# Performance work log

Hardware: AMD Instinct MI355X
Metric: run time of the kernel (lower is better)

Reference implementation:

```python
import jax, jax.numpy as jnp
import numpy as np

NUM_GRAPHS = 64
LEAKY_SLOPE = 0.2
LN_EPS = 1e-5


def setup_inputs() -> dict:
    key = jax.random.key(0)
    ks = jax.random.split(key, 32)
    N, E = 100000, 1600000
    H, C, D = 4, 32, 128
    L = 4
    inp = {}
    inp['x'] = jax.random.normal(ks[0], (N, 8), dtype=jnp.float32)
    inp['edge_index'] = jax.random.randint(ks[1], (2, E), 0, N, dtype=jnp.int64)
    inp['edge_attr'] = jax.random.normal(ks[2], (E, 3), dtype=jnp.float32)
    inp['batch'] = jnp.sort(jax.random.randint(ks[3], (N,), 0, NUM_GRAPHS, dtype=jnp.int64))
    s = 0.05
    inp['node_w'] = jax.random.normal(ks[4], (8, D), dtype=jnp.float32) * s
    inp['node_b'] = jax.random.normal(ks[5], (D,), dtype=jnp.float32) * s
    inp['edge_w'] = jax.random.normal(ks[6], (3, D), dtype=jnp.float32) * s
    inp['edge_b'] = jax.random.normal(ks[7], (D,), dtype=jnp.float32) * s
    inp['gat_lin'] = jax.random.normal(ks[8], (L, D, D), dtype=jnp.float32) * s
    inp['gat_att_src'] = jax.random.normal(ks[9], (L, H, C), dtype=jnp.float32) * s
    inp['gat_att_dst'] = jax.random.normal(ks[10], (L, H, C), dtype=jnp.float32) * s
    inp['gat_lin_edge'] = jax.random.normal(ks[11], (L, D, D), dtype=jnp.float32) * s
    inp['gat_att_edge'] = jax.random.normal(ks[12], (L, H, C), dtype=jnp.float32) * s
    inp['gat_bias'] = jax.random.normal(ks[13], (L, D), dtype=jnp.float32) * s
    inp['ln_g'] = jnp.ones((L, D), dtype=jnp.float32)
    inp['ln_b'] = jnp.zeros((L, D), dtype=jnp.float32)
    inp['dos_w1'] = jax.random.normal(ks[14], (D, D // 2), dtype=jnp.float32) * s
    inp['dos_b1'] = jax.random.normal(ks[15], (D // 2,), dtype=jnp.float32) * s
    inp['dos_w2'] = jax.random.normal(ks[16], (D // 2, 100), dtype=jnp.float32) * s
    inp['dos_b2'] = jax.random.normal(ks[17], (100,), dtype=jnp.float32) * s
    inp['trans_w1'] = jax.random.normal(ks[18], (D, D // 2), dtype=jnp.float32) * s
    inp['trans_b1'] = jax.random.normal(ks[19], (D // 2,), dtype=jnp.float32) * s
    inp['trans_w2'] = jax.random.normal(ks[20], (D // 2, 100), dtype=jnp.float32) * s
    inp['trans_b2'] = jax.random.normal(ks[21], (100,), dtype=jnp.float32) * s
    return inp


def _gat_layer(x, ea, src, dst, lin, a_s, a_d, lin_e, a_e, bias):
    # PyG GATConv (concat=True, add_self_loops=True, fill_value='mean'), eval mode.
    N = x.shape[0]
    H, C = a_s.shape
    h = (x @ lin).reshape(N, H, C)            # [N,H,C]
    # add self loops; self-loop edge_attr = mean of edge_attr over edges
    loop = jnp.arange(N, dtype=src.dtype)
    src_f = jnp.concatenate([src, loop])
    dst_f = jnp.concatenate([dst, loop])
    ea_mean = jnp.broadcast_to(ea.mean(axis=0), (N, ea.shape[1]))
    ea_f = jnp.concatenate([ea, ea_mean], axis=0)
    e = (ea_f @ lin_e).reshape(-1, H, C)      # [E+N,H,C]
    a_src = (h * a_s).sum(-1)                 # [N,H]
    a_dst = (h * a_d).sum(-1)                 # [N,H]
    alpha = a_src[src_f] + a_dst[dst_f] + (e * a_e).sum(-1)  # [E+N,H]
    alpha = jnp.where(alpha >= 0, alpha, LEAKY_SLOPE * alpha)
    # segment softmax over destination nodes
    m = jax.ops.segment_max(alpha, dst_f, num_segments=N)
    ex = jnp.exp(alpha - m[dst_f])
    denom = jax.ops.segment_sum(ex, dst_f, num_segments=N)
    w = ex / (denom[dst_f] + 1e-16)           # [E+N,H]
    msg = h[src_f] * w[:, :, None]            # [E+N,H,C]
    out = jax.ops.segment_sum(msg, dst_f, num_segments=N)
    return out.reshape(N, H * C) + bias


def _layer_norm(x, g, b):
    mu = x.mean(-1, keepdims=True)
    var = ((x - mu) ** 2).mean(-1, keepdims=True)
    return (x - mu) * jax.lax.rsqrt(var + LN_EPS) * g + b


def reference(x, edge_index, edge_attr, batch, node_w, node_b, edge_w, edge_b,
              gat_lin, gat_att_src, gat_att_dst, gat_lin_edge, gat_att_edge,
              gat_bias, ln_g, ln_b, dos_w1, dos_b1, dos_w2, dos_b2,
              trans_w1, trans_b1, trans_w2, trans_b2):
    src, dst = edge_index[0], edge_index[1]
    h = x @ node_w + node_b                   # [N,128]
    ea = edge_attr @ edge_w + edge_b          # [E,128]
    L = gat_lin.shape[0]
    for i in range(L):
        h = _gat_layer(h, ea, src, dst, gat_lin[i], gat_att_src[i],
                       gat_att_dst[i], gat_lin_edge[i], gat_att_edge[i], gat_bias[i])
        h = _layer_norm(h, ln_g[i], ln_b[i])
        h = jax.nn.relu(h)
        # dropout is identity in eval mode
    # global mean pool over graphs
    sums = jax.ops.segment_sum(h, batch, num_segments=NUM_GRAPHS)
    cnts = jax.ops.segment_sum(jnp.ones((h.shape[0], 1), h.dtype), batch, num_segments=NUM_GRAPHS)
    g = sums / jnp.maximum(cnts, 1.0)         # [G,128]
    dos = jax.nn.relu(g @ dos_w1 + dos_b1) @ dos_w2 + dos_b2
    trans = jax.nn.relu(g @ trans_w1 + trans_b1) @ trans_w2 + trans_b2
    return (dos, trans)
```

## Files before the change

kernel.cpp:

```cpp
#include <hip/hip_runtime.h>

#define LEAKY 0.2f
#define LN_EPSV 1e-5f
#define NGRAPH 64

typedef __attribute__((ext_vector_type(8))) short short8v;
typedef __attribute__((ext_vector_type(4))) float f32x4;

static __device__ __forceinline__ float leakyf(float x){ return x >= 0.f ? x : LEAKY*x; }

static __device__ __forceinline__ unsigned short f2bf(float f){
  unsigned int u = __float_as_uint(f);
  u = (u + 0x7fffu + ((u >> 16) & 1u)) >> 16;
  return (unsigned short)u;
}
static __device__ __forceinline__ float bf2f(unsigned short v){
  return __uint_as_float(((unsigned int)v) << 16);
}

__global__ void node_encode_k(const float* __restrict__ x, const float* __restrict__ w,
                              const float* __restrict__ b, unsigned short* __restrict__ hb, int N){
  int tid = blockIdx.x*blockDim.x + threadIdx.x;
  int n = tid >> 5; int c4 = (tid & 31) * 4;
  if (n >= N) return;
  float xr[8];
  #pragma unroll
  for (int k=0;k<8;k++) xr[k] = x[(size_t)n*8+k];
  float4 acc = *(const float4*)&b[c4];
  #pragma unroll
  for (int k=0;k<8;k++){
    float4 wv = *(const float4*)&w[k*128 + c4];
    acc.x += xr[k]*wv.x; acc.y += xr[k]*wv.y; acc.z += xr[k]*wv.z; acc.w += xr[k]*wv.w;
  }
  ushort4 o; o.x=f2bf(acc.x); o.y=f2bf(acc.y); o.z=f2bf(acc.z); o.w=f2bf(acc.w);
  *(ushort4*)&hb[(size_t)n*128 + c4] = o;
}

__global__ void ea_mean_k(const float* __restrict__ ea, float* __restrict__ out, int E){
  float s0=0.f,s1=0.f,s2=0.f;
  for (int e = blockIdx.x*blockDim.x + threadIdx.x; e < E; e += gridDim.x*blockDim.x){
    s0 += ea[(size_t)e*3]; s1 += ea[(size_t)e*3+1]; s2 += ea[(size_t)e*3+2];
  }
  #pragma unroll
  for (int m=32;m;m>>=1){ s0 += __shfl_xor(s0,m); s1 += __shfl_xor(s1,m); s2 += __shfl_xor(s2,m); }
  __shared__ float ls[3][8];
  int wv = threadIdx.x>>6;
  if ((threadIdx.x&63)==0){ ls[0][wv]=s0; ls[1][wv]=s1; ls[2][wv]=s2; }
  __syncthreads();
  if (threadIdx.x==0){
    float a=0.f,b=0.f,c=0.f;
    int nw = blockDim.x>>6;
    for(int i=0;i<nw;i++){ a+=ls[0][i]; b+=ls[1][i]; c+=ls[2][i]; }
    atomicAdd(&out[0],a); atomicAdd(&out[1],b); atomicAdd(&out[2],c);
  }
}

__global__ void csr_count_k(const int* __restrict__ dst, int* __restrict__ cnt, int E){
  int e = blockIdx.x*blockDim.x + threadIdx.x;
  if (e<E) atomicAdd(&cnt[dst[e]], 1);
}

__global__ void scan1_k(const int* __restrict__ in, int* __restrict__ incl, int* __restrict__ bsum, int n){
  __shared__ int s[1024];
  int i = blockIdx.x*1024 + threadIdx.x;
  int v = (i<n)? in[i]:0;
  s[threadIdx.x]=v; __syncthreads();
  for(int off=1;off<1024;off<<=1){
    int t = (threadIdx.x>=off)? s[threadIdx.x-off] : 0;
    __syncthreads();
    s[threadIdx.x]+=t; __syncthreads();
  }
  if(i<n) incl[i]=s[threadIdx.x];
  if(threadIdx.x==1023) bsum[blockIdx.x]=s[1023];
}
__global__ void scan2_k(const int* __restrict__ bsum, int* __restrict__ boff, int nb){
  if(threadIdx.x==0 && blockIdx.x==0){
    int run=0;
    for(int i=0;i<nb;i++){ boff[i]=run; run+=bsum[i]; }
  }
}
__global__ void scan3_k(const int* __restrict__ incl, const int* __restrict__ boff, int* __restrict__ row_ptr, int n){
  int i = blockIdx.x*blockDim.x + threadIdx.x;
  if(i<n) row_ptr[i+1] = incl[i] + boff[i>>10];
  if(i==0) row_ptr[0]=0;
}

__global__ void csr_fill_k(const int* __restrict__ src, const int* __restrict__ dst,
                           const float* __restrict__ eattr,
                           const int* __restrict__ row_ptr, int* __restrict__ cnt,
                           float4* __restrict__ csr_rec, int E){
  int e = blockIdx.x*blockDim.x + threadIdx.x;
  if (e>=E) return;
  int d = dst[e];
  int pos = row_ptr[d] + atomicAdd(&cnt[d],1);
  csr_rec[pos] = make_float4(eattr[(size_t)e*3], eattr[(size_t)e*3+1], eattr[(size_t)e*3+2],
                             __int_as_float(src[e]));
}

__global__ void precompute_k(const float* __restrict__ lin_e, const float* __restrict__ a_e,
                             const float* __restrict__ edge_w, const float* __restrict__ edge_b,
                             const float* __restrict__ emean_sum, float invE,
                             float* __restrict__ params){
  int l = blockIdx.x; int t = threadIdx.x;
  __shared__ float Ve[128][4];
  __shared__ float sW3[12]; __shared__ float sce[4];
  const float* Le = lin_e + (size_t)l*16384; const float* Ae = a_e + l*128;
  #pragma unroll
  for(int h=0; h<4; h++){
    float v=0.f;
    for(int c=0;c<32;c++) v += Le[t*128 + h*32 + c]*Ae[h*32+c];
    Ve[t][h]=v;
  }
  __syncthreads();
  float* P = params + l*32;
  if(t<12){ int k=t>>2, h=t&3; float v=0.f; for(int d=0;d<128;d++) v += edge_w[k*128+d]*Ve[d][h]; P[t]=v; sW3[t]=v; }
  if(t>=16 && t<20){ int h=t-16; float v=0.f; for(int d=0;d<128;d++) v += edge_b[d]*Ve[d][h]; P[12+h]=v; sce[h]=v; }
  __syncthreads();
  if(t<4){
    float v = sce[t];
    for(int k=0;k<3;k++) v += emean_sum[k]*invE * sW3[k*4+t];
    P[16+t]=v;
  }
}

__global__ void prepack_w_k(const float* __restrict__ gat_lin, short8v* __restrict__ wpack){
  int l = blockIdx.x; int t = threadIdx.x;
  const float* W = gat_lin + (size_t)l*16384;
  for(int f = t; f < 2048; f += 256){
    int j = f >> 8, ks = (f >> 6) & 3, lane = f & 63;
    int lo = lane & 15, hi = (lane >> 4) & 3;
    short8v b;
    #pragma unroll
    for(int e=0;e<8;e++) b[e] = (short)f2bf(W[(size_t)(ks*32 + hi*8 + e)*128 + j*16 + lo]);
    wpack[(size_t)l*2048 + f] = b;
  }
}

__global__ __launch_bounds__(256) void mfma_dense_k(const unsigned short* __restrict__ hin,
    const short8v* __restrict__ wpack, const float* __restrict__ att_s, const float* __restrict__ att_d,
    unsigned short* __restrict__ hbf, float* __restrict__ a_src, float* __restrict__ a_dst,
    int N, int ntiles){
  int lane = threadIdx.x & 63;
  int wid  = threadIdx.x >> 6;
  int lo = lane & 15, hi = lane >> 4;
  short8v Bf[8][4];
  #pragma unroll
  for(int j=0;j<8;j++){
    #pragma unroll
    for(int ks=0;ks<4;ks++)
      Bf[j][ks] = wpack[(j<<8) + (ks<<6) + lane];
  }
  float as[8], ad[8];
  #pragma unroll
  for(int j=0;j<8;j++){ as[j]=att_s[j*16+lo]; ad[j]=att_d[j*16+lo]; }

  for(int t = blockIdx.x*4 + wid; t < ntiles; t += gridDim.x*4){
    int n0 = t*16;
    int arow = n0 + lo; if(arow >= N) arow = N-1;
    short8v A[4];
    #pragma unroll
    for(int ks=0;ks<4;ks++)
      A[ks] = *(const short8v*)&hin[(size_t)arow*128 + ks*32 + hi*8];
    float ps[4][4], pd[4][4];
    #pragma unroll
    for(int r=0;r<4;r++){
      #pragma unroll
      for(int h=0;h<4;h++){ ps[r][h]=0.f; pd[r][h]=0.f; }
    }
    #pragma unroll
    for(int j=0;j<8;j++){
      f32x4 acc = {0.f,0.f,0.f,0.f};
      #pragma unroll
      for(int ks=0;ks<4;ks++)
        acc = __builtin_amdgcn_mfma_f32_16x16x32_bf16(A[ks], Bf[j][ks], acc, 0, 0, 0);
      int h = j>>1;
      #pragma unroll
      for(int r=0;r<4;r++){
        int row = n0 + hi*4 + r;
        if(row < N) hbf[(size_t)row*128 + j*16 + lo] = f2bf(acc[r]);
        ps[r][h] += acc[r]*as[j];
        pd[r][h] += acc[r]*ad[j];
      }
    }
    #pragma unroll
    for(int r=0;r<4;r++){
      #pragma unroll
      for(int h=0;h<4;h++){
        #pragma unroll
        for(int msk=1; msk<16; msk<<=1){
          ps[r][h] += __shfl_xor(ps[r][h], msk);
          pd[r][h] += __shfl_xor(pd[r][h], msk);
        }
      }
    }
    if(lo==0){
      #pragma unroll
      for(int r=0;r<4;r++){
        int row = n0 + hi*4 + r;
        if(row<N){
          *(float4*)&a_src[(size_t)row*4] = make_float4(ps[r][0],ps[r][1],ps[r][2],ps[r][3]);
          *(float4*)&a_dst[(size_t)row*4] = make_float4(pd[r][0],pd[r][1],pd[r][2],pd[r][3]);
        }
      }
    }
  }
}

__global__ void aggregate_k(const unsigned int* __restrict__ hbf, const float* __restrict__ a_src,
    const float* __restrict__ a_dst, const int* __restrict__ row_ptr,
    const float4* __restrict__ csr_rec, const float* __restrict__ params,
    const float* __restrict__ bias, const float* __restrict__ lng, const float* __restrict__ lnb,
    unsigned int* __restrict__ h_out, int N){
  int lane = threadIdx.x & 63;
  int n = blockIdx.x*(blockDim.x>>6) + (threadIdx.x>>6);
  if(n>=N) return;
  int g  = lane >> 4;
  int eh = lane & 3;
  int ee = lane >> 2;
  float W0 = params[eh], W1 = params[4+eh], W2 = params[8+eh];
  float ce = params[12+eh], aes = params[16+eh];
  float adst = a_dst[n*4+eh];
  float m = leakyf(a_src[n*4+eh] + adst + aes);
  float dpart = (ee==0) ? 1.f : 0.f;
  float2 acc;
  {
    unsigned int u = hbf[(size_t)n*64 + lane];
    acc.x = __uint_as_float(u << 16);
    acc.y = __uint_as_float(u & 0xffff0000u);
  }
  int s = row_ptr[n], e = row_ptr[n+1];
  for(int base=s; base<e; base+=16){
    int nv = e - base; if(nv>16) nv=16;
    int sr = 0; float4 rc = make_float4(0.f,0.f,0.f,0.f);
    if(ee < nv){
      rc = csr_rec[base+ee];
      sr = __float_as_int(rc.w);
    }
    float asr = (ee < nv) ? a_src[sr*4+eh] : 0.f;
    unsigned int u[16];
    #pragma unroll
    for(int q=0;q<16;q++){
      int srq = __shfl(sr, q*4);
      u[q] = hbf[(size_t)srq*64 + lane];
    }
    float al = -1e30f;
    if(ee < nv) al = leakyf(asr + adst + rc.x*W0 + rc.y*W1 + rc.z*W2 + ce);
    float cm = al;
    cm = fmaxf(cm, __shfl_xor(cm,4));
    cm = fmaxf(cm, __shfl_xor(cm,8));
    cm = fmaxf(cm, __shfl_xor(cm,16));
    cm = fmaxf(cm, __shfl_xor(cm,32));
    float nm = fmaxf(m, cm);
    float sc = __expf(m - nm);
    float p  = __expf(al - nm);
    dpart = dpart*sc + p;
    m = nm;
    float scg = __shfl(sc, g);
    acc.x *= scg; acc.y *= scg;
    #pragma unroll
    for(int q=0;q<16;q++){
      float pq = __shfl(p, q*4 + g);
      float hx = __uint_as_float(u[q] << 16);
      float hy = __uint_as_float(u[q] & 0xffff0000u);
      acc.x += pq*hx; acc.y += pq*hy;
    }
  }
  float dsum = dpart;
  dsum += __shfl_xor(dsum,4);
  dsum += __shfl_xor(dsum,8);
  dsum += __shfl_xor(dsum,16);
  dsum += __shfl_xor(dsum,32);
  float inv = 1.f/(__shfl(dsum, g) + 1e-16f);
  int c = lane*2;
  float ox = acc.x*inv + bias[c], oy = acc.y*inv + bias[c+1];
  float sum = ox+oy;
  #pragma unroll
  for(int msk=32;msk;msk>>=1) sum += __shfl_xor(sum,msk);
  float mean = sum*(1.f/128.f);
  float dx = ox-mean, dy = oy-mean;
  float sq = dx*dx + dy*dy;
  #pragma unroll
  for(int msk=32;msk;msk>>=1) sq += __shfl_xor(sq,msk);
  float r = rsqrtf(sq*(1.f/128.f) + LN_EPSV);
  float yx = fmaxf(dx*r*lng[c]  + lnb[c],   0.f);
  float yy = fmaxf(dy*r*lng[c+1]+ lnb[c+1], 0.f);
  h_out[(size_t)n*64 + lane] = (unsigned int)f2bf(yx) | ((unsigned int)f2bf(yy) << 16);
}

__global__ void pool_k(const unsigned short* __restrict__ h, const int* __restrict__ batch,
                       float* __restrict__ sums, float* __restrict__ cntf, int N){
  int t = threadIdx.x;
  int n0 = blockIdx.x*256;
  int nend = n0+256; if (nend > N) nend = N;
  float acc = 0.f; float runc = 0.f; int curb = -1;
  for(int n=n0;n<nend;n++){
    int b = batch[n];
    if(b!=curb){
      if(curb>=0){ atomicAdd(&sums[curb*128+t], acc); if(t==0) atomicAdd(&cntf[curb], runc); }
      acc=0.f; runc=0.f; curb=b;
    }
    acc += bf2f(h[(size_t)n*128+t]);
    runc += 1.f;
  }
  if(curb>=0){ atomicAdd(&sums[curb*128+t], acc); if(t==0) atomicAdd(&cntf[curb], runc); }
}

__global__ void heads_k(const float* __restrict__ sums, const float* __restrict__ cntf,
    const float* __restrict__ w1a, const float* __restrict__ b1a,
    const float* __restrict__ w2a, const float* __restrict__ b2a,
    const float* __restrict__ w1b, const float* __restrict__ b1b,
    const float* __restrict__ w2b, const float* __restrict__ b2b,
    float* __restrict__ out){
  int g = blockIdx.x, t = threadIdx.x;
  __shared__ float gv[128]; __shared__ float hid[64];
  float c = fmaxf(cntf[g], 1.f);
  gv[t] = sums[g*128+t] / c;
  __syncthreads();
  if(t<64){ float v=b1a[t]; for(int d=0;d<128;d++) v += gv[d]*w1a[d*64+t]; hid[t]=fmaxf(v,0.f); }
  __syncthreads();
  if(t<100){ float v=b2a[t]; for(int j=0;j<64;j++) v += hid[j]*w2a[j*100+t]; out[g*100+t]=v; }
  __syncthreads();
  if(t<64){ float v=b1b[t]; for(int d=0;d<128;d++) v += gv[d]*w1b[d*64+t]; hid[t]=fmaxf(v,0.f); }
  __syncthreads();
  if(t<100){ float v=b2b[t]; for(int j=0;j<64;j++) v += hid[j]*w2b[j*100+t]; out[6400 + g*100+t]=v; }
}

extern "C" void kernel_launch(void* const* d_in, const int* in_sizes, int n_in,
                              void* d_out, int out_size, void* d_ws, size_t ws_size,
                              hipStream_t stream){
  const float* x      = (const float*)d_in[0];
  const int*   ei     = (const int*)d_in[1];
  const float* eattr  = (const float*)d_in[2];
  const int*   batch  = (const int*)d_in[3];
  const float* node_w = (const float*)d_in[4];
  const float* node_b = (const float*)d_in[5];
  const float* edge_w = (const float*)d_in[6];
  const float* edge_b = (const float*)d_in[7];
  const float* gat_lin= (const float*)d_in[8];
  const float* att_s  = (const float*)d_in[9];
  const float* att_d  = (const float*)d_in[10];
  const float* lin_e  = (const float*)d_in[11];
  const float* att_e  = (const float*)d_in[12];
  const float* gat_bias=(const float*)d_in[13];
  const float* ln_g   = (const float*)d_in[14];
  const float* ln_b   = (const float*)d_in[15];

  const int N = in_sizes[0]/8;
  const int E = in_sizes[2]/3;
  const int* srcp = ei;
  const int* dstp = ei + E;

  char* wp = (char*)d_ws;
  auto alloc = [&](size_t bytes)->char*{ char* p = wp; wp += (bytes+255)&~(size_t)255; return p; };
  unsigned short* hb_node  = (unsigned short*) alloc((size_t)N*128*2);
  unsigned short* hbf_tab  = (unsigned short*) alloc((size_t)N*128*2);
  float*  a_srcb  = (float*) alloc((size_t)N*4*4);
  float*  a_dstb  = (float*) alloc((size_t)N*4*4);
  int*    row_ptr = (int*)   alloc((size_t)(N+1)*4);
  int*    cnt     = (int*)   alloc((size_t)N*4);
  float4* csr_rec = (float4*)alloc((size_t)E*16);
  int*    incl    = (int*)   alloc((size_t)N*4);
  int     nb      = (N+1023)/1024;
  int*    bsum    = (int*)   alloc((size_t)nb*4);
  int*    boff    = (int*)   alloc((size_t)nb*4);
  float*  emean   = (float*) alloc(16);
  float*  params  = (float*) alloc(4*32*4);
  float*  psums   = (float*) alloc(64*128*4);
  float*  pcnt    = (float*) alloc(64*4);
  short8v* wpack  = (short8v*)alloc((size_t)4*2048*16);
  (void)ws_size; (void)n_in; (void)out_size;

  hipMemsetAsync(cnt, 0, (size_t)N*4, stream);
  hipMemsetAsync(emean, 0, 16, stream);
  hipMemsetAsync(psums, 0, 64*128*4, stream);
  hipMemsetAsync(pcnt, 0, 64*4, stream);

  node_encode_k<<<(N*32+255)/256, 256, 0, stream>>>(x, node_w, node_b, hb_node, N);
  ea_mean_k<<<1024, 256, 0, stream>>>(eattr, emean, E);
  csr_count_k<<<(E+255)/256, 256, 0, stream>>>(dstp, cnt, E);
  scan1_k<<<nb, 1024, 0, stream>>>(cnt, incl, bsum, N);
  scan2_k<<<1, 64, 0, stream>>>(bsum, boff, nb);
  scan3_k<<<(N+255)/256, 256, 0, stream>>>(incl, boff, row_ptr, N);
  hipMemsetAsync(cnt, 0, (size_t)N*4, stream);
  csr_fill_k<<<(E+255)/256, 256, 0, stream>>>(srcp, dstp, eattr, row_ptr, cnt, csr_rec, E);
  precompute_k<<<4, 128, 0, stream>>>(lin_e, att_e, edge_w, edge_b, emean, 1.0f/(float)E, params);
  prepack_w_k<<<4, 256, 0, stream>>>(gat_lin, wpack);

  int ntiles = (N+15)/16;
  for(int l=0;l<4;l++){
    mfma_dense_k<<<1024, 256, 0, stream>>>(hb_node, wpack + (size_t)l*2048,
        att_s + l*128, att_d + l*128, hbf_tab, a_srcb, a_dstb, N, ntiles);
    aggregate_k<<<(N+3)/4, 256, 0, stream>>>((const unsigned int*)hbf_tab, a_srcb, a_dstb,
        row_ptr, csr_rec,
        params + l*32, gat_bias + l*128, ln_g + l*128, ln_b + l*128,
        (unsigned int*)hb_node, N);
  }

  pool_k<<<(N+255)/256, 128, 0, stream>>>(hb_node, batch, psums, pcnt, N);
  heads_k<<<64, 128, 0, stream>>>(psums, pcnt,
      (const float*)d_in[16], (const float*)d_in[17], (const float*)d_in[18], (const float*)d_in[19],
      (const float*)d_in[20], (const float*)d_in[21], (const float*)d_in[22], (const float*)d_in[23],
      (float*)d_out);
}
```

Baseline: 911.6 us.

## Fuse front-end kernels, vectorize CSR fill, process 32 edges per aggregate chunk

Merges node encoding, the edge-attribute mean and the CSR degree count into one grid-stride kernel, cutting launches and extra passes over the edge arrays. CSR fill now handles four edges per thread with vectorized loads of edge attributes, src and dst. The aggregate kernel processes 32 edges per iteration instead of 16 and issues 32 gathered row loads before accumulating, to expose more memory-level parallelism. The trade-off is higher register pressure in aggregate and the loss of per-kernel occupancy tuning in the fused front kernel.

```diff
diff --git a/kernel.cpp b/kernel.cpp
--- a/kernel.cpp
+++ b/kernel.cpp
@@ -18,28 +18,30 @@
   return __uint_as_float(((unsigned int)v) << 16);
 }
 
-__global__ void node_encode_k(const float* __restrict__ x, const float* __restrict__ w,
-                              const float* __restrict__ b, unsigned short* __restrict__ hb, int N){
-  int tid = blockIdx.x*blockDim.x + threadIdx.x;
-  int n = tid >> 5; int c4 = (tid & 31) * 4;
-  if (n >= N) return;
-  float xr[8];
-  #pragma unroll
-  for (int k=0;k<8;k++) xr[k] = x[(size_t)n*8+k];
-  float4 acc = *(const float4*)&b[c4];
-  #pragma unroll
-  for (int k=0;k<8;k++){
-    float4 wv = *(const float4*)&w[k*128 + c4];
-    acc.x += xr[k]*wv.x; acc.y += xr[k]*wv.y; acc.z += xr[k]*wv.z; acc.w += xr[k]*wv.w;
-  }
-  ushort4 o; o.x=f2bf(acc.x); o.y=f2bf(acc.y); o.z=f2bf(acc.z); o.w=f2bf(acc.w);
-  *(ushort4*)&hb[(size_t)n*128 + c4] = o;
-}
-
-__global__ void ea_mean_k(const float* __restrict__ ea, float* __restrict__ out, int E){
+__global__ void front_k(const float* __restrict__ x, const float* __restrict__ w,
+                        const float* __restrict__ b, unsigned short* __restrict__ hb, int N,
+                        const float* __restrict__ ea, float* __restrict__ emean,
+                        const int* __restrict__ dst, int* __restrict__ cnt, int E){
+  int stride = gridDim.x*blockDim.x;
+  int tid0 = blockIdx.x*blockDim.x + threadIdx.x;
+  for(int tid = tid0; tid < N*32; tid += stride){
+    int n = tid >> 5; int c4 = (tid & 31) * 4;
+    float xr[8];
+    #pragma unroll
+    for (int k=0;k<8;k++) xr[k] = x[(size_t)n*8+k];
+    float4 acc = *(const float4*)&b[c4];
+    #pragma unroll
+    for (int k=0;k<8;k++){
+      float4 wv = *(const float4*)&w[k*128 + c4];
+      acc.x += xr[k]*wv.x; acc.y += xr[k]*wv.y; acc.z += xr[k]*wv.z; acc.w += xr[k]*wv.w;
+    }
+    ushort4 o; o.x=f2bf(acc.x); o.y=f2bf(acc.y); o.z=f2bf(acc.z); o.w=f2bf(acc.w);
+    *(ushort4*)&hb[(size_t)n*128 + c4] = o;
+  }
   float s0=0.f,s1=0.f,s2=0.f;
-  for (int e = blockIdx.x*blockDim.x + threadIdx.x; e < E; e += gridDim.x*blockDim.x){
+  for (int e = tid0; e < E; e += stride){
     s0 += ea[(size_t)e*3]; s1 += ea[(size_t)e*3+1]; s2 += ea[(size_t)e*3+2];
+    atomicAdd(&cnt[dst[e]], 1);
   }
   #pragma unroll
   for (int m=32;m;m>>=1){ s0 += __shfl_xor(s0,m); s1 += __shfl_xor(s1,m); s2 += __shfl_xor(s2,m); }
@@ -48,16 +50,11 @@
   if ((threadIdx.x&63)==0){ ls[0][wv]=s0; ls[1][wv]=s1; ls[2][wv]=s2; }
   __syncthreads();
   if (threadIdx.x==0){
-    float a=0.f,b=0.f,c=0.f;
+    float a=0.f,bb=0.f,c=0.f;
     int nw = blockDim.x>>6;
-    for(int i=0;i<nw;i++){ a+=ls[0][i]; b+=ls[1][i]; c+=ls[2][i]; }
-    atomicAdd(&out[0],a); atomicAdd(&out[1],b); atomicAdd(&out[2],c);
-  }
-}
-
-__global__ void csr_count_k(const int* __restrict__ dst, int* __restrict__ cnt, int E){
-  int e = blockIdx.x*blockDim.x + threadIdx.x;
-  if (e<E) atomicAdd(&cnt[dst[e]], 1);
+    for(int i=0;i<nw;i++){ a+=ls[0][i]; bb+=ls[1][i]; c+=ls[2][i]; }
+    atomicAdd(&emean[0],a); atomicAdd(&emean[1],bb); atomicAdd(&emean[2],c);
+  }
 }
 
 __global__ void scan1_k(const int* __restrict__ in, int* __restrict__ incl, int* __restrict__ bsum, int n){
@@ -89,12 +86,30 @@
                            const float* __restrict__ eattr,
                            const int* __restrict__ row_ptr, int* __restrict__ cnt,
                            float4* __restrict__ csr_rec, int E){
-  int e = blockIdx.x*blockDim.x + threadIdx.x;
-  if (e>=E) return;
-  int d = dst[e];
-  int pos = row_ptr[d] + atomicAdd(&cnt[d],1);
-  csr_rec[pos] = make_float4(eattr[(size_t)e*3], eattr[(size_t)e*3+1], eattr[(size_t)e*3+2],
-                             __int_as_float(src[e]));
+  int t = blockIdx.x*blockDim.x + threadIdx.x;
+  int e0 = t*4;
+  if (e0+3 < E){
+    float4 a0 = *(const float4*)&eattr[(size_t)e0*3];
+    float4 a1 = *(const float4*)&eattr[(size_t)e0*3+4];
+    float4 a2 = *(const float4*)&eattr[(size_t)e0*3+8];
+    int4 d4 = *(const int4*)&dst[e0];
+    int4 s4 = *(const int4*)&src[e0];
+    int p0 = row_ptr[d4.x] + atomicAdd(&cnt[d4.x],1);
+    int p1 = row_ptr[d4.y] + atomicAdd(&cnt[d4.y],1);
+    int p2 = row_ptr[d4.z] + atomicAdd(&cnt[d4.z],1);
+    int p3 = row_ptr[d4.w] + atomicAdd(&cnt[d4.w],1);
+    csr_rec[p0] = make_float4(a0.x,a0.y,a0.z, __int_as_float(s4.x));
+    csr_rec[p1] = make_float4(a0.w,a1.x,a1.y, __int_as_float(s4.y));
+    csr_rec[p2] = make_float4(a1.z,a1.w,a2.x, __int_as_float(s4.z));
+    csr_rec[p3] = make_float4(a2.y,a2.z,a2.w, __int_as_float(s4.w));
+  } else {
+    for(int e=e0; e<E; ++e){
+      int d = dst[e];
+      int pos = row_ptr[d] + atomicAdd(&cnt[d],1);
+      csr_rec[pos] = make_float4(eattr[(size_t)e*3], eattr[(size_t)e*3+1], eattr[(size_t)e*3+2],
+                                 __int_as_float(src[e]));
+    }
+  }
 }
 
 __global__ void precompute_k(const float* __restrict__ lin_e, const float* __restrict__ a_e,
@@ -229,39 +244,55 @@
     acc.y = __uint_as_float(u & 0xffff0000u);
   }
   int s = row_ptr[n], e = row_ptr[n+1];
-  for(int base=s; base<e; base+=16){
-    int nv = e - base; if(nv>16) nv=16;
-    int sr = 0; float4 rc = make_float4(0.f,0.f,0.f,0.f);
+  for(int base=s; base<e; base+=32){
+    int nv = e - base; if(nv>32) nv=32;
+    int sra = 0, srb = 0; float ala = -1e30f, alb = -1e30f;
     if(ee < nv){
-      rc = csr_rec[base+ee];
-      sr = __float_as_int(rc.w);
-    }
-    float asr = (ee < nv) ? a_src[sr*4+eh] : 0.f;
-    unsigned int u[16];
-    #pragma unroll
-    for(int q=0;q<16;q++){
-      int srq = __shfl(sr, q*4);
-      u[q] = hbf[(size_t)srq*64 + lane];
-    }
-    float al = -1e30f;
-    if(ee < nv) al = leakyf(asr + adst + rc.x*W0 + rc.y*W1 + rc.z*W2 + ce);
-    float cm = al;
+      float4 rc = csr_rec[base+ee];
+      sra = __float_as_int(rc.w);
+      ala = leakyf(a_src[sra*4+eh] + adst + rc.x*W0 + rc.y*W1 + rc.z*W2 + ce);
+    }
+    if(ee+16 < nv){
+      float4 rc = csr_rec[base+ee+16];
+      srb = __float_as_int(rc.w);
+      alb = leakyf(a_src[srb*4+eh] + adst + rc.x*W0 + rc.y*W1 + rc.z*W2 + ce);
+    }
+    float cm = fmaxf(ala, alb);
     cm = fmaxf(cm, __shfl_xor(cm,4));
     cm = fmaxf(cm, __shfl_xor(cm,8));
     cm = fmaxf(cm, __shfl_xor(cm,16));
     cm = fmaxf(cm, __shfl_xor(cm,32));
     float nm = fmaxf(m, cm);
     float sc = __expf(m - nm);
-    float p  = __expf(al - nm);
-    dpart = dpart*sc + p;
+    float pa = __expf(ala - nm);
+    float pb = __expf(alb - nm);
+    dpart = dpart*sc + pa + pb;
     m = nm;
+    unsigned int u[32];
+    #pragma unroll
+    for(int q=0;q<16;q++){
+      int srq = __shfl(sra, q*4);
+      u[q] = hbf[(size_t)srq*64 + lane];
+    }
+    #pragma unroll
+    for(int q=0;q<16;q++){
+      int srq = __shfl(srb, q*4);
+      u[16+q] = hbf[(size_t)srq*64 + lane];
+    }
     float scg = __shfl(sc, g);
     acc.x *= scg; acc.y *= scg;
     #pragma unroll
     for(int q=0;q<16;q++){
-      float pq = __shfl(p, q*4 + g);
+      float pq = __shfl(pa, q*4 + g);
       float hx = __uint_as_float(u[q] << 16);
       float hy = __uint_as_float(u[q] & 0xffff0000u);
+      acc.x += pq*hx; acc.y += pq*hy;
+    }
+    #pragma unroll
+    for(int q=0;q<16;q++){
+      float pq = __shfl(pb, q*4 + g);
+      float hx = __uint_as_float(u[16+q] << 16);
+      float hy = __uint_as_float(u[16+q] & 0xffff0000u);
       acc.x += pq*hx; acc.y += pq*hy;
     }
   }
@@ -375,14 +406,12 @@
   hipMemsetAsync(psums, 0, 64*128*4, stream);
   hipMemsetAsync(pcnt, 0, 64*4, stream);
 
-  node_encode_k<<<(N*32+255)/256, 256, 0, stream>>>(x, node_w, node_b, hb_node, N);
-  ea_mean_k<<<1024, 256, 0, stream>>>(eattr, emean, E);
-  csr_count_k<<<(E+255)/256, 256, 0, stream>>>(dstp, cnt, E);
+  front_k<<<2048, 256, 0, stream>>>(x, node_w, node_b, hb_node, N, eattr, emean, dstp, cnt, E);
   scan1_k<<<nb, 1024, 0, stream>>>(cnt, incl, bsum, N);
   scan2_k<<<1, 64, 0, stream>>>(bsum, boff, nb);
   scan3_k<<<(N+255)/256, 256, 0, stream>>>(incl, boff, row_ptr, N);
   hipMemsetAsync(cnt, 0, (size_t)N*4, stream);
-  csr_fill_k<<<(E+255)/256, 256, 0, stream>>>(srcp, dstp, eattr, row_ptr, cnt, csr_rec, E);
+  csr_fill_k<<<((E+3)/4+255)/256, 256, 0, stream>>>(srcp, dstp, eattr, row_ptr, cnt, csr_rec, E);
   precompute_k<<<4, 128, 0, stream>>>(lin_e, att_e, edge_w, edge_b, emean, 1.0f/(float)E, params);
   prepack_w_k<<<4, 256, 0, stream>>>(gat_lin, wpack);
 
```

Result: faster. 873.5 us (-4.2%).
